# Performance work log

Measured on AMD Instinct MI355X. Metric: run time of the kernel, lower is better.

## Reference

```python
import jax, jax.numpy as jnp
import numpy as np

LAMBDA = 20.0   # lambda_val (blackbox-diff smoothing)
REG = 0.5       # reg
MAX_LABEL = 8   # labels drawn in [0, MAX_LABEL)


def _pairwise_dist(x):
    # x: [n, d] -> [n, n] euclidean distances (safe sqrt, exact 0 on diagonal)
    sq = jnp.sum(x * x, axis=-1)
    d2 = sq[:, None] + sq[None, :] - 2.0 * (x @ x.T)
    d2 = jnp.maximum(d2, 0.0)
    return jnp.where(d2 > 0, jnp.sqrt(jnp.where(d2 > 0, d2, 1.0)), 0.0)


def _single_linkage_adj(D, k):
    # Agglomerative (single-linkage) clustering of n points given [n,n] dists,
    # stopped at k clusters; returns [n,n] 0/1 cluster-adjacency matrix.
    n = D.shape[0]
    BIG = jnp.asarray(1e9, D.dtype)
    eye = jnp.eye(n, dtype=bool)
    Dw0 = jnp.where(eye, BIG, D)
    labels0 = jnp.arange(n)
    active0 = jnp.ones((n,), dtype=bool)

    def step(carry, _):
        Dw, labels, active = carry
        mask = active[:, None] & active[None, :] & ~eye
        flat = jnp.argmin(jnp.where(mask, Dw, BIG))
        i, j = flat // n, flat % n
        a = jnp.minimum(i, j)
        b = jnp.maximum(i, j)
        newrow = jnp.minimum(Dw[a], Dw[b])        # single linkage merge
        Dw = Dw.at[a, :].set(newrow).at[:, a].set(newrow)
        active = active.at[b].set(False)
        labels = jnp.where(labels == b, a, labels)
        return (Dw, labels, active), labels

    _, hist = jax.lax.scan(step, (Dw0, labels0, active0), None, length=n - 1)
    all_hist = jnp.concatenate([labels0[None, :], hist], axis=0)  # [n, n]; row m = labels after m merges (n-m clusters)
    lab = all_hist[n - k]
    return (lab[:, None] == lab[None, :]).astype(D.dtype)


def _solve(dists, ks):
    return jax.vmap(_single_linkage_adj)(dists, ks)


def setup_inputs() -> dict:
    key = jax.random.key(0)
    k1, k2, k3 = jax.random.split(key, 3)
    B, n, d = 256, 64, 768
    return {
        "query_embedding": jax.random.normal(k1, (B, d), dtype=jnp.float32),
        "psg_embeddings": jax.random.normal(k2, (B, n, d), dtype=jnp.float32),
        "labels": jax.random.randint(k3, (B, n), 0, MAX_LABEL, dtype=jnp.int64)
        if jax.config.jax_enable_x64 else jax.random.randint(k3, (B, n), 0, MAX_LABEL, dtype=jnp.int32),
    }


def reference(query_embedding, psg_embeddings, labels):
    # true_adj_mat: adj[i,j] = 1 iff i==j or label[i]==label[j] (diag is label-equal anyway)
    true_adj = (labels[:, :, None] == labels[:, None, :]).astype(jnp.float32)  # [B,n,n]
    # ks[i] = number of unique labels in sample i
    presence = (labels[..., None] == jnp.arange(MAX_LABEL)).any(axis=1)  # [B, MAX_LABEL]
    ks = presence.sum(axis=-1)

    scaled = query_embedding[:, None, :] * psg_embeddings            # [B,n,d]
    dists = jax.vmap(_pairwise_dist)(scaled)                          # [B,n,n]

    mean_similar = (dists * true_adj).sum() / true_adj.sum()
    mean_dissimilar = (dists * (1.0 - true_adj)).sum() / (1.0 - true_adj).sum()

    adj = _solve(dists, ks)                                           # OptimCluster forward
    err = adj * (1.0 - true_adj) + (1.0 - adj) * true_adj
    err_mean = err.mean(axis=0).sum()
    return err_mean + REG * (mean_similar - mean_dissimilar)
```

## Files before the change

### kernel.cpp

```cpp
#include <hip/hip_runtime.h>


#define NPTS 64
#define DIM 768
#define CH 128
#define NCH 6
#define NT 512
#define BIGF 1e9f
#define PGS 68

typedef __attribute__((ext_vector_type(8))) __bf16 bf16x8;
typedef __attribute__((ext_vector_type(4))) float f32x4;
typedef __attribute__((ext_vector_type(8))) unsigned short us8;

__device__ __forceinline__ void lds_fence() {
  asm volatile("s_waitcnt lgkmcnt(0)" ::: "memory");
  __builtin_amdgcn_sched_barrier(0);
}

__device__ __forceinline__ void split3(float x, unsigned short& h,
                                       unsigned short& m, unsigned short& l) {
  unsigned u = __float_as_uint(x);
  unsigned rb = (u + 0x7FFFu + ((u >> 16) & 1u)) & 0xFFFF0000u;
  h = (unsigned short)(rb >> 16);
  float r1 = x - __uint_as_float(rb);
  unsigned u1 = __float_as_uint(r1);
  unsigned rb1 = (u1 + 0x7FFFu + ((u1 >> 16) & 1u)) & 0xFFFF0000u;
  m = (unsigned short)(rb1 >> 16);
  float r2 = r1 - __uint_as_float(rb1);
  l = (unsigned short)(__float_as_uint(r2) >> 16);
}

__device__ __forceinline__ unsigned long long match6(int v) {
  unsigned long long m = ~0ull;
  #pragma unroll
  for (int bb = 0; bb < 6; ++bb) {
    unsigned long long mb = __ballot(((v >> bb) & 1) != 0);
    m &= (((v >> bb) & 1) != 0) ? mb : ~mb;
  }
  return m;
}

__device__ __forceinline__ void stage_chunk(
    unsigned short (*Hb)[NPTS][CH], const float4 (&pva)[2][2],
    const float4 (&qv)[2], int row0, int gran) {
  #pragma unroll
  for (int rr = 0; rr < 2; ++rr) {
    const int row = row0 + (rr << 5);
    float xs[8];
    xs[0] = pva[rr][0].x * qv[0].x; xs[1] = pva[rr][0].y * qv[0].y;
    xs[2] = pva[rr][0].z * qv[0].z; xs[3] = pva[rr][0].w * qv[0].w;
    xs[4] = pva[rr][1].x * qv[1].x; xs[5] = pva[rr][1].y * qv[1].y;
    xs[6] = pva[rr][1].z * qv[1].z; xs[7] = pva[rr][1].w * qv[1].w;
    us8 uh, um, ul;
    #pragma unroll
    for (int e = 0; e < 8; ++e) {
      unsigned short hh, mm, ll;
      split3(xs[e], hh, mm, ll);
      uh[e] = hh; um[e] = mm; ul[e] = ll;
    }
    const int p = gran ^ (row & 15);
    *reinterpret_cast<us8*>(&Hb[0][row][p << 3]) = uh;
    *reinterpret_cast<us8*>(&Hb[1][row][p << 3]) = um;
    *reinterpret_cast<us8*>(&Hb[2][row][p << 3]) = ul;
  }
}

__device__ __forceinline__ void mfma_chunk(
    const unsigned short (*Hb)[NPTS][CH], f32x4 (&acc)[2][2],
    int R, int C, int ksub, int lrow, int lhi) {
  #pragma unroll 1
  for (int ss = 0; ss < 2; ++ss) {
    const int s = ksub + (ss << 1);
    const int p = ((s << 2) + lhi) ^ lrow;
    bf16x8 fa[3][2], fb[3][2];
    #pragma unroll
    for (int v = 0; v < 3; ++v)
      #pragma unroll
      for (int tb = 0; tb < 2; ++tb) {
        const int row = (R << 5) + (tb << 4) + lrow;
        fa[v][tb] = *reinterpret_cast<const bf16x8*>(&Hb[v][row][p << 3]);
      }
    if (R != C) {
      #pragma unroll
      for (int v = 0; v < 3; ++v)
        #pragma unroll
        for (int tb = 0; tb < 2; ++tb) {
          const int row = (C << 5) + (tb << 4) + lrow;
          fb[v][tb] = *reinterpret_cast<const bf16x8*>(&Hb[v][row][p << 3]);
        }
    } else {
      #pragma unroll
      for (int v = 0; v < 3; ++v)
        #pragma unroll
        for (int tb = 0; tb < 2; ++tb) fb[v][tb] = fa[v][tb];
    }
    #pragma unroll
    for (int ti = 0; ti < 2; ++ti)
      #pragma unroll
      for (int tj = 0; tj < 2; ++tj) {
        acc[ti][tj] = __builtin_amdgcn_mfma_f32_16x16x32_bf16(fa[0][ti], fb[0][tj], acc[ti][tj], 0, 0, 0);
        acc[ti][tj] = __builtin_amdgcn_mfma_f32_16x16x32_bf16(fa[0][ti], fb[1][tj], acc[ti][tj], 0, 0, 0);
        acc[ti][tj] = __builtin_amdgcn_mfma_f32_16x16x32_bf16(fa[1][ti], fb[0][tj], acc[ti][tj], 0, 0, 0);
        acc[ti][tj] = __builtin_amdgcn_mfma_f32_16x16x32_bf16(fa[1][ti], fb[1][tj], acc[ti][tj], 0, 0, 0);
        acc[ti][tj] = __builtin_amdgcn_mfma_f32_16x16x32_bf16(fa[0][ti], fb[2][tj], acc[ti][tj], 0, 0, 0);
        acc[ti][tj] = __builtin_amdgcn_mfma_f32_16x16x32_bf16(fa[2][ti], fb[0][tj], acc[ti][tj], 0, 0, 0);
      }
  }
}

#define ISSUE_P(PV, cix) do {                                       \
    const int off_ = (cix) * CH;                                    \
    PV[0][0] = *(const float4*)(pr0 + off_);                        \
    PV[0][1] = *(const float4*)(pr0 + off_ + 4);                    \
    PV[1][0] = *(const float4*)(pr1 + off_);                        \
    PV[1][1] = *(const float4*)(pr1 + off_ + 4);                    \
  } while (0)

#define ISSUE_Q(QV, cix) do {                                       \
    const int off_ = (cix) * CH;                                    \
    QV[0] = *(const float4*)(qr + off_);                            \
    QV[1] = *(const float4*)(qr + off_ + 4);                        \
  } while (0)

__global__ __launch_bounds__(NT) void fused_kernel(
    const float* __restrict__ q,
    const float* __restrict__ psg,
    const int*   __restrict__ labels,
    float* __restrict__ simS_o, float* __restrict__ disS_o,
    int* __restrict__ simC_o, int* __restrict__ errC_o)
{
  __shared__ __align__(16) unsigned short Hml[2][3][NPTS][CH];
  __shared__ __align__(16) float PG[NPTS * PGS];
  __shared__ float diagf[NPTS];
  __shared__ unsigned bw_s[NPTS], bfl_s[NPTS];
  __shared__ int lab_s[NPTS];
  __shared__ __align__(8) unsigned long long ekey_s[NPTS];

  const int b = blockIdx.x;
  const int t = threadIdx.x;
  const int w = t >> 6;
  const int l = t & 63;

  const float* qb = q + (size_t)b * DIM;
  const float* pb = psg + (size_t)b * NPTS * DIM;

  const int row0 = t >> 4;
  const int gran = t & 15;
  const float* pr0 = pb + (size_t)row0 * DIM + (gran << 3);
  const float* pr1 = pr0 + 32 * DIM;
  const float* qr  = qb + (gran << 3);

  const int rw = w >> 1;
  const int R = rw >> 1, C = rw & 1;
  const int ksub = w & 1;
  const int lrow = l & 15;
  const int lhi  = l >> 4;

  f32x4 acc[2][2];
  {
    f32x4 z = {0.f, 0.f, 0.f, 0.f};
    acc[0][0] = z; acc[0][1] = z; acc[1][0] = z; acc[1][1] = z;
  }

  float4 pvaA[2][2], pvaB[2][2], qv[2];

  ISSUE_P(pvaA, 0);
  ISSUE_Q(qv, 0);
  ISSUE_P(pvaB, 1);
  stage_chunk(Hml[0], pvaA, qv, row0, gran);
  __syncthreads();

  #pragma unroll 1
  for (int cc = 0; cc < 3; ++cc) {
    if (cc < 2) ISSUE_P(pvaA, 2 * cc + 2);
    ISSUE_Q(qv, 2 * cc + 1);
    mfma_chunk(Hml[0], acc, R, C, ksub, lrow, lhi);
    stage_chunk(Hml[1], pvaB, qv, row0, gran);
    __syncthreads();
    if (cc < 2) {
      ISSUE_P(pvaB, 2 * cc + 3);
      ISSUE_Q(qv, 2 * cc + 2);
    }
    mfma_chunk(Hml[1], acc, R, C, ksub, lrow, lhi);
    if (cc < 2) stage_chunk(Hml[0], pvaA, qv, row0, gran);
    __syncthreads();
  }

  if (w & 1) {
    float* dst = PG + (rw << 10);
    #pragma unroll
    for (int ti = 0; ti < 2; ++ti)
      #pragma unroll
      for (int tj = 0; tj < 2; ++tj)
        *reinterpret_cast<f32x4*>(dst + (((ti << 1) + tj) << 8) + (l << 2)) = acc[ti][tj];
  }
  __syncthreads();
  if (!(w & 1)) {
    const float* src = PG + (rw << 10);
    #pragma unroll
    for (int ti = 0; ti < 2; ++ti)
      #pragma unroll
      for (int tj = 0; tj < 2; ++tj)
        acc[ti][tj] += *reinterpret_cast<const f32x4*>(src + (((ti << 1) + tj) << 8) + (l << 2));
  }
  __syncthreads();
  if (!(w & 1)) {
    #pragma unroll
    for (int ti = 0; ti < 2; ++ti)
      #pragma unroll
      for (int tj = 0; tj < 2; ++tj)
        #pragma unroll
        for (int reg = 0; reg < 4; ++reg) {
          const int grow = (R << 5) + (ti << 4) + (lhi << 2) + reg;
          const int gcol = (C << 5) + (tj << 4) + lrow;
          PG[grow * PGS + gcol] = acc[ti][tj][reg];
        }
  }
  __syncthreads();

  if (t < NPTS) diagf[t] = PG[t * PGS + t];
  __syncthreads();
  {
    const int r  = t >> 3;
    const int c0 = (t & 7) << 3;
    const float dr = diagf[r];
    #pragma unroll
    for (int e = 0; e < 8; ++e) {
      const int cc = c0 + e;
      const float gg = PG[r * PGS + cc];
      float d2 = dr + diagf[cc] - 2.f * gg;
      d2 = fmaxf(d2, 0.f);
      PG[r * PGS + cc] = (d2 > 0.f) ? sqrtf(d2) : 0.f;
    }
  }
  __syncthreads();
  if (w != 0) return;

  float drow[64];
  #pragma unroll
  for (int v4 = 0; v4 < 16; ++v4) {
    f32x4 x = *reinterpret_cast<const f32x4*>(&PG[l * PGS + (v4 << 2)]);
    drow[v4 * 4 + 0] = x[0]; drow[v4 * 4 + 1] = x[1];
    drow[v4 * 4 + 2] = x[2]; drow[v4 * 4 + 3] = x[3];
  }
  int tl = labels[b * NPTS + l];

  unsigned long long sMask = 0ull;
  int kcnt = 0;
  #pragma unroll
  for (int v = 0; v < 8; ++v) {
    unsigned long long mv = __ballot(tl == v);
    kcnt += (mv != 0ull) ? 1 : 0;
    if (tl == v) sMask = mv;
  }
  int simC = __popcll(sMask);
  const int merges = NPTS - kcnt;

  float simS = 0.f, disS = 0.f;
  #pragma unroll
  for (int j = 0; j < NPTS; ++j) {
    bool sim = (sMask >> j) & 1ull;
    simS += sim ? drow[j] : 0.f;
    disS += sim ? 0.f : drow[j];
  }

  unsigned long long same = 1ull << l;
  int repSlot = l;
  int ecnt = 0;

  #pragma unroll 1
  for (int rd = 0; rd < 6; ++rd) {
    bw_s[l] = 0xFFFFFFFFu; bfl_s[l] = 0xFFFFFFFFu;
    lds_fence();
    float bv = BIGF; int bj = 64;
    #pragma unroll
    for (int j = 0; j < NPTS; ++j) {
      bool ok = !((same >> j) & 1ull) && (drow[j] < bv);
      bv = ok ? drow[j] : bv;
      bj = ok ? j : bj;
    }
    if (bj < 64) atomicMin(&bw_s[repSlot], __float_as_uint(bv));
    lds_fence();
    const unsigned bwc = bw_s[repSlot];
    if (bj < 64 && __float_as_uint(bv) == bwc)
      atomicMin(&bfl_s[repSlot], (unsigned)((l << 6) | bj));
    lds_fence();
    const unsigned rfl = bfl_s[repSlot];
    const bool valid = (bwc != 0xFFFFFFFFu);
    const int vpt = (int)(rfl & 63);
    const int otherRep = __shfl(repSlot, vpt);
    const bool isRoot = (l == repSlot);
    int ptr = repSlot;
    if (isRoot && valid) ptr = otherRep;
    const int pd = __shfl(ptr, ptr);
    bool adder = false;
    if (isRoot && valid && ptr != l) {
      if (pd == l && l < ptr) ptr = l;
      else adder = true;
    }
    const unsigned long long A = __ballot(adder);
    if (adder)
      ekey_s[ecnt + __popcll(A & ((1ull << l) - 1ull))] =
          ((unsigned long long)bwc << 12) | (unsigned long long)rfl;
    ecnt += (int)__popcll(A);
    #pragma unroll 1
    for (int jj = 0; jj < 6; ++jj) {
      const int p2 = __shfl(ptr, ptr);
      if (__ballot(p2 != ptr) == 0ull) break;
      ptr = p2;
    }
    same = match6(ptr);
    repSlot = __ffsll((long long)same) - 1;
    if (same == ~0ull) break;
  }
  lds_fence();

  const bool ehave = (l < ecnt);
  const unsigned long long my = ehave ? ekey_s[l] : ~0ull;
  int rank = 0;
  #pragma unroll 7
  for (int j = 0; j < 63; ++j) {
    unsigned long long kj = ekey_s[j];
    rank += (j < ecnt && kj < my) ? 1 : 0;
  }
  const bool kept = ehave && (rank < merges);
  const int eu = (int)((my >> 6) & 63);
  const int ev = (int)(my & 63);

  lab_s[l] = l;
  lds_fence();
  #pragma unroll 1
  for (int iter = 0; iter < 64; ++iter) {
    int m = 0; bool ch = false;
    if (kept) {
      const int lu = lab_s[eu], lv = lab_s[ev];
      m = min(lu, lv);
      ch = (m < lu) || (m < lv);
    }
    if (ch) {
      atomicMin(&lab_s[eu], m);
      atomicMin(&lab_s[ev], m);
    }
    lds_fence();
    const int la = lab_s[l];
    const int lb = lab_s[la];
    if (lb < la) lab_s[l] = lb;
    lds_fence();
    if (__ballot(ch) == 0ull) break;
  }
  const int cl = lab_s[l];

  const unsigned long long cMask = match6(cl);
  int ec2 = __popcll(cMask ^ sMask);

  #pragma unroll
  for (int off = 32; off; off >>= 1) {
    simS += __shfl_xor(simS, off);
    disS += __shfl_xor(disS, off);
    simC += __shfl_xor(simC, off);
    ec2  += __shfl_xor(ec2, off);
  }
  if (l == 0) {
    simS_o[b] = simS; disS_o[b] = disS;
    simC_o[b] = simC; errC_o[b] = ec2;
  }
}

__global__ __launch_bounds__(64) void finalize_kernel(
    const float* __restrict__ simS, const float* __restrict__ disS,
    const int* __restrict__ simC, const int* __restrict__ errC,
    float* __restrict__ out)
{
  const int l = threadIdx.x;
  double ss = 0.0, dd = 0.0, sc = 0.0, ec = 0.0;
  #pragma unroll
  for (int r = 0; r < 4; ++r) {
    int i = (r << 6) + l;
    ss += (double)simS[i];
    dd += (double)disS[i];
    sc += (double)simC[i];
    ec += (double)errC[i];
  }
  #pragma unroll
  for (int off = 32; off; off >>= 1) {
    ss += __shfl_xor(ss, off);
    dd += __shfl_xor(dd, off);
    sc += __shfl_xor(sc, off);
    ec += __shfl_xor(ec, off);
  }
  if (l == 0) {
    const double total = 256.0 * 4096.0;
    double ms = ss / sc;
    double md = dd / (total - sc);
    out[0] = (float)(ec / 256.0 + 0.5 * (ms - md));
  }
}

extern "C" void kernel_launch(void* const* d_in, const int* in_sizes, int n_in,
                              void* d_out, int out_size, void* d_ws, size_t ws_size,
                              hipStream_t stream) {
  const float* q      = (const float*)d_in[0];
  const float* psg    = (const float*)d_in[1];
  const int*   labels = (const int*)d_in[2];
  float* out = (float*)d_out;

  float* simS = (float*)d_ws;
  float* disS = simS + 256;
  int*   simC = (int*)(disS + 256);
  int*   errC = simC + 256;

  fused_kernel<<<256, NT, 0, stream>>>(q, psg, labels, simS, disS, simC, errC);
  finalize_kernel<<<1, 64, 0, stream>>>(simS, disS, simC, errC, out);
}
```

Before: 32.13 us.

## Drop third bf16 split term and replace LDS atomics with ballot-based reductions

The pairwise Gram matrix now uses a two-term bf16 split (hi/mid) instead of three terms. This cuts the MFMA count per tile from 6 to 4, shrinks the LDS staging buffers by a third and reduces staging work. The Boruvka-style merge rounds drop LDS atomicMin and fences. They find per-component minimum edges with a 32-step ballot bit-serial min, and replace shfl lookups with ballot-published 6-bit values. The lower precision may perturb distances enough to change near-tie merge decisions, and the ballot loops add ALU work in place of the LDS round trips.

After: 31.79 us. About the same (-1.1%).

```diff
diff --git a/kernel.cpp b/kernel.cpp
--- a/kernel.cpp
+++ b/kernel.cpp
@@ -18,8 +18,8 @@
   __builtin_amdgcn_sched_barrier(0);
 }
 
-__device__ __forceinline__ void split3(float x, unsigned short& h,
-                                       unsigned short& m, unsigned short& l) {
+__device__ __forceinline__ void split2(float x, unsigned short& h,
+                                       unsigned short& m) {
   unsigned u = __float_as_uint(x);
   unsigned rb = (u + 0x7FFFu + ((u >> 16) & 1u)) & 0xFFFF0000u;
   h = (unsigned short)(rb >> 16);
@@ -27,10 +27,18 @@
   unsigned u1 = __float_as_uint(r1);
   unsigned rb1 = (u1 + 0x7FFFu + ((u1 >> 16) & 1u)) & 0xFFFF0000u;
   m = (unsigned short)(rb1 >> 16);
-  float r2 = r1 - __uint_as_float(rb1);
-  l = (unsigned short)(__float_as_uint(r2) >> 16);
-}
-
+}
+
+__device__ __forceinline__ void publish6(int v, unsigned long long (&m)[6]) {
+  #pragma unroll
+  for (int k = 0; k < 6; ++k) m[k] = __ballot(((v >> k) & 1) != 0);
+}
+__device__ __forceinline__ int extract6(const unsigned long long (&m)[6], int p) {
+  int r = 0;
+  #pragma unroll
+  for (int k = 0; k < 6; ++k) r |= (int)((m[k] >> p) & 1ull) << k;
+  return r;
+}
 __device__ __forceinline__ unsigned long long match6(int v) {
   unsigned long long m = ~0ull;
   #pragma unroll
@@ -52,17 +60,16 @@
     xs[2] = pva[rr][0].z * qv[0].z; xs[3] = pva[rr][0].w * qv[0].w;
     xs[4] = pva[rr][1].x * qv[1].x; xs[5] = pva[rr][1].y * qv[1].y;
     xs[6] = pva[rr][1].z * qv[1].z; xs[7] = pva[rr][1].w * qv[1].w;
-    us8 uh, um, ul;
+    us8 uh, um;
     #pragma unroll
     for (int e = 0; e < 8; ++e) {
-      unsigned short hh, mm, ll;
-      split3(xs[e], hh, mm, ll);
-      uh[e] = hh; um[e] = mm; ul[e] = ll;
+      unsigned short hh, mm;
+      split2(xs[e], hh, mm);
+      uh[e] = hh; um[e] = mm;
     }
     const int p = gran ^ (row & 15);
     *reinterpret_cast<us8*>(&Hb[0][row][p << 3]) = uh;
     *reinterpret_cast<us8*>(&Hb[1][row][p << 3]) = um;
-    *reinterpret_cast<us8*>(&Hb[2][row][p << 3]) = ul;
   }
 }
 
@@ -73,9 +80,9 @@
   for (int ss = 0; ss < 2; ++ss) {
     const int s = ksub + (ss << 1);
     const int p = ((s << 2) + lhi) ^ lrow;
-    bf16x8 fa[3][2], fb[3][2];
-    #pragma unroll
-    for (int v = 0; v < 3; ++v)
+    bf16x8 fa[2][2], fb[2][2];
+    #pragma unroll
+    for (int v = 0; v < 2; ++v)
       #pragma unroll
       for (int tb = 0; tb < 2; ++tb) {
         const int row = (R << 5) + (tb << 4) + lrow;
@@ -83,7 +90,7 @@
       }
     if (R != C) {
       #pragma unroll
-      for (int v = 0; v < 3; ++v)
+      for (int v = 0; v < 2; ++v)
         #pragma unroll
         for (int tb = 0; tb < 2; ++tb) {
           const int row = (C << 5) + (tb << 4) + lrow;
@@ -91,7 +98,7 @@
         }
     } else {
       #pragma unroll
-      for (int v = 0; v < 3; ++v)
+      for (int v = 0; v < 2; ++v)
         #pragma unroll
         for (int tb = 0; tb < 2; ++tb) fb[v][tb] = fa[v][tb];
     }
@@ -103,8 +110,6 @@
         acc[ti][tj] = __builtin_amdgcn_mfma_f32_16x16x32_bf16(fa[0][ti], fb[1][tj], acc[ti][tj], 0, 0, 0);
         acc[ti][tj] = __builtin_amdgcn_mfma_f32_16x16x32_bf16(fa[1][ti], fb[0][tj], acc[ti][tj], 0, 0, 0);
         acc[ti][tj] = __builtin_amdgcn_mfma_f32_16x16x32_bf16(fa[1][ti], fb[1][tj], acc[ti][tj], 0, 0, 0);
-        acc[ti][tj] = __builtin_amdgcn_mfma_f32_16x16x32_bf16(fa[0][ti], fb[2][tj], acc[ti][tj], 0, 0, 0);
-        acc[ti][tj] = __builtin_amdgcn_mfma_f32_16x16x32_bf16(fa[2][ti], fb[0][tj], acc[ti][tj], 0, 0, 0);
       }
   }
 }
@@ -130,10 +135,9 @@
     float* __restrict__ simS_o, float* __restrict__ disS_o,
     int* __restrict__ simC_o, int* __restrict__ errC_o)
 {
-  __shared__ __align__(16) unsigned short Hml[2][3][NPTS][CH];
+  __shared__ __align__(16) unsigned short Hml[2][2][NPTS][CH];
   __shared__ __align__(16) float PG[NPTS * PGS];
   __shared__ float diagf[NPTS];
-  __shared__ unsigned bw_s[NPTS], bfl_s[NPTS];
   __shared__ int lab_s[NPTS];
   __shared__ __align__(8) unsigned long long ekey_s[NPTS];
 
@@ -271,29 +275,51 @@
 
   #pragma unroll 1
   for (int rd = 0; rd < 6; ++rd) {
-    bw_s[l] = 0xFFFFFFFFu; bfl_s[l] = 0xFFFFFFFFu;
-    lds_fence();
-    float bv = BIGF; int bj = 64;
-    #pragma unroll
-    for (int j = 0; j < NPTS; ++j) {
-      bool ok = !((same >> j) & 1ull) && (drow[j] < bv);
-      bv = ok ? drow[j] : bv;
-      bj = ok ? j : bj;
-    }
-    if (bj < 64) atomicMin(&bw_s[repSlot], __float_as_uint(bv));
-    lds_fence();
-    const unsigned bwc = bw_s[repSlot];
-    if (bj < 64 && __float_as_uint(bv) == bwc)
-      atomicMin(&bfl_s[repSlot], (unsigned)((l << 6) | bj));
-    lds_fence();
-    const unsigned rfl = bfl_s[repSlot];
-    const bool valid = (bwc != 0xFFFFFFFFu);
-    const int vpt = (int)(rfl & 63);
-    const int otherRep = __shfl(repSlot, vpt);
+    float bva = BIGF, bvb = BIGF, bvc = BIGF, bvd = BIGF;
+    int bja = 64, bjb = 64, bjc = 64, bjd = 64;
+    #pragma unroll
+    for (int j4 = 0; j4 < 16; ++j4) {
+      const int j = j4 << 2;
+      bool oa = !((same >> (j + 0)) & 1ull) && (drow[j + 0] < bva);
+      bva = oa ? drow[j + 0] : bva; bja = oa ? j + 0 : bja;
+      bool ob = !((same >> (j + 1)) & 1ull) && (drow[j + 1] < bvb);
+      bvb = ob ? drow[j + 1] : bvb; bjb = ob ? j + 1 : bjb;
+      bool oc = !((same >> (j + 2)) & 1ull) && (drow[j + 2] < bvc);
+      bvc = oc ? drow[j + 2] : bvc; bjc = oc ? j + 2 : bjc;
+      bool od = !((same >> (j + 3)) & 1ull) && (drow[j + 3] < bvd);
+      bvd = od ? drow[j + 3] : bvd; bjd = od ? j + 3 : bjd;
+    }
+    float bv = bva; int bj = bja;
+    if (bvb < bv || (bvb == bv && bjb < bj)) { bv = bvb; bj = bjb; }
+    if (bvc < bv || (bvc == bv && bjc < bj)) { bv = bvc; bj = bjc; }
+    if (bvd < bv || (bvd == bv && bjd < bj)) { bv = bvd; bj = bjd; }
+
+    const unsigned bits = (bj < 64) ? __float_as_uint(bv) : 0xFFFFFFFFu;
+    unsigned long long cand = same;
+    unsigned minb = 0u;
+    #pragma unroll
+    for (int k = 31; k >= 0; --k) {
+      unsigned long long mb = __ballot(((bits >> k) & 1u) != 0u);
+      unsigned long long z = cand & ~mb;
+      bool hz = (z != 0ull);
+      cand = hz ? z : cand;
+      minb = (minb << 1) | (hz ? 0u : 1u);
+    }
+    const bool valid = (minb != 0xFFFFFFFFu);
+    const int wl = __ffsll((long long)cand) - 1;
+
+    unsigned long long bjm[6]; publish6(bj, bjm);
+    const int v_wl = extract6(bjm, wl);
+
+    unsigned long long rpm[6]; publish6(repSlot, rpm);
+    const int otherRep = extract6(rpm, v_wl);
+
     const bool isRoot = (l == repSlot);
     int ptr = repSlot;
     if (isRoot && valid) ptr = otherRep;
-    const int pd = __shfl(ptr, ptr);
+
+    unsigned long long pm[6]; publish6(ptr, pm);
+    const int pd = extract6(pm, ptr);
     bool adder = false;
     if (isRoot && valid && ptr != l) {
       if (pd == l && l < ptr) ptr = l;
@@ -302,11 +328,14 @@
     const unsigned long long A = __ballot(adder);
     if (adder)
       ekey_s[ecnt + __popcll(A & ((1ull << l) - 1ull))] =
-          ((unsigned long long)bwc << 12) | (unsigned long long)rfl;
+          ((unsigned long long)minb << 12) |
+          (unsigned long long)((wl << 6) | v_wl);
     ecnt += (int)__popcll(A);
+
     #pragma unroll 1
     for (int jj = 0; jj < 6; ++jj) {
-      const int p2 = __shfl(ptr, ptr);
+      unsigned long long dm[6]; publish6(ptr, dm);
+      const int p2 = extract6(dm, ptr);
       if (__ballot(p2 != ptr) == 0ull) break;
       ptr = p2;
     }
```
